# Performance work log

Measured on AMD Instinct MI355X. Metric: run time of the kernel, lower is better.

The kernel has to match this reference:

```python
import jax, jax.numpy as jnp
import numpy as np

B, N, DIM, VDIM, H, HD = 4, 1369, 1024, 1536, 16, 64
ROPE_HW, ROPE_DIM, THETA = 37, 32, 10000.0
LN_EPS = 1e-5


def _rope_tables():
    # VisionRotaryEmbeddingFast: freqs_for='lang', dim=32, pt_seq_len=ft_seq_len=37
    inv = 1.0 / THETA ** (jnp.arange(0, ROPE_DIM, 2, dtype=jnp.float32) / ROPE_DIM)  # [16]
    t = jnp.arange(ROPE_HW, dtype=jnp.float32) / ROPE_HW * ROPE_HW                    # [37]
    f = t[:, None] * inv[None, :]                                                     # [37,16]
    f = jnp.repeat(f, 2, axis=-1)                                                     # [37,32]
    # broadcat along last dim over the 2D grid -> [37,37,64]
    f2 = jnp.concatenate([jnp.broadcast_to(f[:, None, :], (ROPE_HW, ROPE_HW, ROPE_DIM)),
                          jnp.broadcast_to(f[None, :, :], (ROPE_HW, ROPE_HW, ROPE_DIM))], axis=-1)
    f2 = f2.reshape(-1, 2 * ROPE_DIM)                                                 # [1369,64]
    return jnp.cos(f2), jnp.sin(f2)


def _rotate_half(x):
    # pairs (x0,x1) -> (-x1,x0), interleaved
    xr = x.reshape(*x.shape[:-1], x.shape[-1] // 2, 2)
    x1, x2 = xr[..., 0], xr[..., 1]
    return jnp.stack((-x2, x1), axis=-1).reshape(x.shape)


def setup_inputs() -> dict:
    key = jax.random.key(0)
    ks = jax.random.split(key, 8)
    return {
        "x": jax.random.normal(ks[0], (B, N, DIM), jnp.float32),
        "value": jax.random.normal(ks[1], (B, N, VDIM), jnp.float32),
        "attn_mask": jax.random.randint(ks[2], (B, N), 0, 2).astype(bool),
        "wq": jax.random.normal(ks[3], (DIM, DIM), jnp.float32) * 0.02,
        "wk": jax.random.normal(ks[4], (DIM, VDIM), jnp.float32) * 0.02,
        "wv": jax.random.normal(ks[5], (DIM, VDIM), jnp.float32) * 0.02,
        "ln_g": jnp.ones((DIM,), jnp.float32),
        "ln_b": jnp.zeros((DIM,), jnp.float32),
        "wp": jax.random.normal(ks[6], (DIM, DIM), jnp.float32) * 0.02,
        "bp": jnp.zeros((DIM,), jnp.float32),
    }


def reference(x, value, attn_mask, wq, wk, wv, ln_g, ln_b, wp, bp):
    cos, sin = _rope_tables()  # [N, 64] each
    # projections (torch F.linear: y = x @ W.T)
    q = jnp.einsum('bni,oi->bno', x, wq).reshape(B, N, H, HD).transpose(0, 2, 1, 3)
    k = jnp.einsum('bni,oi->bno', value, wk).reshape(B, N, H, HD).transpose(0, 2, 1, 3)
    v = jnp.einsum('bni,oi->bno', value, wv).reshape(B, N, H, HD).transpose(0, 2, 1, 3)
    # inline RoPE on q and k
    q = q * cos + _rotate_half(q) * sin
    k = k * cos + _rotate_half(k) * sin
    q = q * (HD ** -0.5)
    attn = jnp.einsum('bhnd,bhmd->bhnm', q, k)
    neg_inf = jnp.finfo(attn.dtype).min
    attn = jnp.where(attn_mask[:, None, None, :], attn, neg_inf)
    attn = jax.nn.softmax(attn, axis=-1)
    out = jnp.einsum('bhnm,bhmd->bhnd', attn, v)
    out = out.transpose(0, 2, 1, 3).reshape(B, N, H * HD)
    # inner_attn_ln (LayerNorm, eps=1e-5)
    mu = jnp.mean(out, axis=-1, keepdims=True)
    var = jnp.var(out, axis=-1, keepdims=True)
    out = (out - mu) * jax.lax.rsqrt(var + LN_EPS) * ln_g + ln_b
    # output projection
    return jnp.einsum('bni,oi->bno', out, wp) + bp
```

## Files before the change

kernel.cpp:

```cpp
#include <hip/hip_runtime.h>
#include <hip/hip_bf16.h>

#define BB 4
#define NN 1369
#define DIMM 1024
#define VDIMM 1536
#define HH 16
#define MM (BB*NN)
#define MPAD 5504
#define NPAD 1408
#define KVB 64
#define NT (NPAD/KVB)
#define QSCALE 0.18028334f

typedef __attribute__((ext_vector_type(4))) float f32x4;
typedef __attribute__((ext_vector_type(8))) __bf16 bf16x8;
typedef __attribute__((ext_vector_type(4))) __bf16 bf16x4;

#define GLOAD_LDS(gsrc, ldst) \
  __builtin_amdgcn_global_load_lds((const __attribute__((address_space(1))) unsigned int*)(gsrc), \
                                   (__attribute__((address_space(3))) unsigned int*)(ldst), 16, 0, 0)

__global__ __launch_bounds__(256) void cvt_inputs(const float* __restrict__ x,
                                                  const float* __restrict__ val,
                                                  __bf16* __restrict__ xb,
                                                  __bf16* __restrict__ vb) {
  const int NX = MM * 1024 / 4;
  const int NV = MM * 1536 / 4;
  int i = blockIdx.x * blockDim.x + threadIdx.x;
  int st = gridDim.x * blockDim.x;
  for (; i < NX + NV; i += st) {
    const float* s; __bf16* d; int j;
    if (i < NX) { s = x; d = xb; j = i; }
    else        { s = val; d = vb; j = i - NX; }
    f32x4 v = ((const f32x4*)s)[j];
    bf16x4 o;
    o[0] = (__bf16)v[0]; o[1] = (__bf16)v[1];
    o[2] = (__bf16)v[2]; o[3] = (__bf16)v[3];
    ((bf16x4*)d)[j] = o;
  }
}

__global__ __launch_bounds__(256) void cvt_weights(
    const float* __restrict__ wq, const float* __restrict__ wk,
    const float* __restrict__ wv, const float* __restrict__ wp,
    const float* __restrict__ g,
    __bf16* __restrict__ wqb, __bf16* __restrict__ wkvb, __bf16* __restrict__ wgb) {
  const int NQ = 1024 * 1024 / 4;
  const int NK = 1024 * 1536 / 4;
  int i = blockIdx.x * blockDim.x + threadIdx.x;
  int st = gridDim.x * blockDim.x;
  for (; i < 2 * NQ + 2 * NK; i += st) {
    int j = i;
    if (j < NQ) {
      f32x4 v = ((const f32x4*)wq)[j];
      bf16x4 o;
      o[0] = (__bf16)v[0]; o[1] = (__bf16)v[1]; o[2] = (__bf16)v[2]; o[3] = (__bf16)v[3];
      ((bf16x4*)wqb)[j] = o;
    } else if (j < NQ + NK) {
      j -= NQ;
      f32x4 v = ((const f32x4*)wk)[j];
      bf16x4 o;
      o[0] = (__bf16)v[0]; o[1] = (__bf16)v[1]; o[2] = (__bf16)v[2]; o[3] = (__bf16)v[3];
      ((bf16x4*)wkvb)[j] = o;
    } else if (j < NQ + 2 * NK) {
      j -= NQ + NK;
      f32x4 v = ((const f32x4*)wv)[j];
      bf16x4 o;
      o[0] = (__bf16)v[0]; o[1] = (__bf16)v[1]; o[2] = (__bf16)v[2]; o[3] = (__bf16)v[3];
      ((bf16x4*)(wkvb + (size_t)1024 * 1536))[j] = o;
    } else {
      j -= NQ + 2 * NK;
      f32x4 v = ((const f32x4*)wp)[j];
      f32x4 gv = ((const f32x4*)g)[j & 255];
      bf16x4 o;
      o[0] = (__bf16)(v[0] * gv[0]); o[1] = (__bf16)(v[1] * gv[1]);
      o[2] = (__bf16)(v[2] * gv[2]); o[3] = (__bf16)(v[3] * gv[3]);
      ((bf16x4*)wgb)[j] = o;
    }
  }
}

__global__ __launch_bounds__(256) void c12_kernel(
    const float* __restrict__ wp, const float* __restrict__ g,
    const float* __restrict__ lnb, const float* __restrict__ bpv,
    float* __restrict__ c1, float* __restrict__ c2) {
  const int w = threadIdx.x >> 6, l = threadIdx.x & 63;
  const int o = blockIdx.x * 4 + w;
  const float* row = wp + (size_t)o * 1024;
  float s1 = 0.f, s2 = 0.f;
#pragma unroll
  for (int j = 0; j < 4; ++j) {
    const int idx = l * 4 + j * 256;
    f32x4 wv = *(const f32x4*)&row[idx];
    f32x4 gv = *(const f32x4*)&g[idx];
    f32x4 bv = *(const f32x4*)&lnb[idx];
#pragma unroll
    for (int e = 0; e < 4; ++e) { s1 += wv[e] * gv[e]; s2 += wv[e] * bv[e]; }
  }
#pragma unroll
  for (int m = 1; m < 64; m <<= 1) { s1 += __shfl_xor(s1, m); s2 += __shfl_xor(s2, m); }
  if (l == 0) { c1[o] = s1; c2[o] = s2 + bpv[o]; }
}

__global__ __launch_bounds__(256) void stats_kernel(
    const __bf16* __restrict__ AO, float* __restrict__ mu, float* __restrict__ rstd) {
  const int w = threadIdx.x >> 6, l = threadIdx.x & 63;
  const int row = blockIdx.x * 4 + w;
  const __bf16* x = AO + (size_t)row * DIMM + l * 16;
  float s = 0.f, sq = 0.f;
#pragma unroll
  for (int j = 0; j < 2; ++j) {
    bf16x8 v = *(const bf16x8*)&x[j * 8];
#pragma unroll
    for (int e = 0; e < 8; ++e) { float f = (float)v[e]; s += f; sq += f * f; }
  }
#pragma unroll
  for (int m = 1; m < 64; m <<= 1) { s += __shfl_xor(s, m); sq += __shfl_xor(sq, m); }
  if (l == 0) {
    float mean = s * (1.f / 1024.f);
    mu[row] = mean;
    rstd[row] = rsqrtf(sq * (1.f / 1024.f) - mean * mean + 1e-5f);
  }
}

__global__ __launch_bounds__(256) void prep_aux(float* __restrict__ cosT,
                                                float* __restrict__ sinT,
                                                const void* __restrict__ mask,
                                                float* __restrict__ maskA) {
  const int blk = blockIdx.x;
  if (blk < 343) {
    int idx = blk * 256 + threadIdx.x;
    if (idx >= NN * 64) return;
    int n = idx >> 6, d = idx & 63;
    int r = n / 37, c = n % 37;
    int m = (d < 32) ? (d >> 1) : ((d - 32) >> 1);
    float p = (d < 32) ? (float)r : (float)c;
    float inv = powf(10000.f, -(float)m * (1.f / 16.f));
    float a = p * inv;
    cosT[idx] = cosf(a);
    sinT[idx] = sinf(a);
  } else {
    __shared__ int flags[2];
    int t = threadIdx.x;
    if (t < 2) flags[t] = 0;
    __syncthreads();
    const unsigned int* mw = (const unsigned int*)mask;
    for (int i = t; i < NN; i += blockDim.x) {
      unsigned int w = mw[i];
      if (w == 0x3F800000u) atomicOr(&flags[1], 1);
      else if (w > 1u) atomicOr(&flags[0], 1);
    }
    __syncthreads();
    int md = flags[1] ? 2 : (flags[0] ? 1 : 0);
    const unsigned char* mb = (const unsigned char*)mask;
    const float* mf = (const float*)mask;
    for (int i = t; i < BB * NPAD; i += blockDim.x) {
      int b = i / NPAD, key = i % NPAD;
      float v = -1e30f;
      if (key < NN) {
        int idx = b * NN + key;
        bool on = (md == 0) ? (mw[idx] != 0u) : (md == 1) ? (mb[idx] != 0) : (mf[idx] != 0.f);
        if (on) v = 0.f;
      }
      maskA[i] = v;
    }
  }
}

template <int TN, int EPI, int GRID2D>
__global__ __launch_bounds__(256) void gemm_bt(
    const __bf16* __restrict__ A, const __bf16* __restrict__ W, int K,
    __bf16* __restrict__ obf, __bf16* __restrict__ obf2, float* __restrict__ of32,
    const float* __restrict__ cosT, const float* __restrict__ sinT,
    const float* __restrict__ mu, const float* __restrict__ rstd,
    const float* __restrict__ c1, const float* __restrict__ c2) {
  constexpr int MI = (TN == 128) ? 4 : 2;
  __shared__ __bf16 As[2][128 * 32];
  __shared__ __bf16 Bs[2][TN * 32];
  const int tid = threadIdx.x;
  const int w = tid >> 6, l = tid & 63;
  int tN, tM;
  if (GRID2D) {
    tN = blockIdx.x; tM = blockIdx.y;
  } else {
    const int i0 = blockIdx.x;
    const int orig = (i0 & 7) * 86 + (i0 >> 3);
    tN = orig & 15; tM = orig >> 4;
  }
  const int wm = (TN == 128) ? (w >> 1) : w;
  const int wn = (TN == 128) ? (w & 1) : 0;
  const int wmo = wm * ((TN == 128) ? 64 : 32);
  const int lo = l & 15, hi = l >> 4;

  const __bf16* Asrc = A + (size_t)(tM * 128 + lo) * K + hi * 8;
  const __bf16* Wsrc = W + (size_t)(tN * TN + lo) * K + hi * 8;

  f32x4 zero = {0.f, 0.f, 0.f, 0.f};
  f32x4 acc[MI][4];
#pragma unroll
  for (int i = 0; i < MI; ++i)
#pragma unroll
    for (int j = 0; j < 4; ++j) acc[i][j] = zero;

  auto GSTAGE = [&](int buf, int k0) {
#pragma unroll
    for (int j = 0; j < 2; ++j) {
      const int c = j * 4 + w;
      GLOAD_LDS(Asrc + (size_t)c * 16 * K + k0, (char*)&As[buf][c * 512]);
    }
    if constexpr (TN == 128) {
#pragma unroll
      for (int j = 0; j < 2; ++j) {
        const int c = j * 4 + w;
        GLOAD_LDS(Wsrc + (size_t)c * 16 * K + k0, (char*)&Bs[buf][c * 512]);
      }
    } else {
      GLOAD_LDS(Wsrc + (size_t)w * 16 * K + k0, (char*)&Bs[buf][w * 512]);
    }
  };

  const int nk = K >> 5;
  GSTAGE(0, 0);
  int cur = 0;
  const int ga = wmo >> 4;
  const int gb = (TN == 128) ? (wn * 4) : 0;
  for (int t = 0; t < nk; ++t) {
    __syncthreads();
    if (t + 1 < nk) GSTAGE(cur ^ 1, (t + 1) * 32);
    bf16x8 af[MI], bfr[4];
#pragma unroll
    for (int mi = 0; mi < MI; ++mi)
      af[mi] = *(const bf16x8*)&As[cur][(ga + mi) * 512 + hi * 128 + lo * 8];
#pragma unroll
    for (int ni = 0; ni < 4; ++ni)
      bfr[ni] = *(const bf16x8*)&Bs[cur][(gb + ni) * 512 + hi * 128 + lo * 8];
    __builtin_amdgcn_s_setprio(1);
#pragma unroll
    for (int mi = 0; mi < MI; ++mi)
#pragma unroll
      for (int ni = 0; ni < 4; ++ni)
        acc[mi][ni] = __builtin_amdgcn_mfma_f32_16x16x32_bf16(af[mi], bfr[ni], acc[mi][ni], 0, 0, 0);
    __builtin_amdgcn_s_setprio(0);
    cur ^= 1;
  }

  const int m_base = tM * 128 + wmo;
  const int o_base = tN * TN + wn * 64;
  const bool isK = (EPI == 1) && (tN < 8);
  float c1v[4], c2v[4];
  if (EPI == 3) {
#pragma unroll
    for (int ni = 0; ni < 4; ++ni) {
      c1v[ni] = c1[o_base + ni * 16 + lo];
      c2v[ni] = c2[o_base + ni * 16 + lo];
    }
  }
#pragma unroll
  for (int mi = 0; mi < MI; ++mi) {
    const int m4 = m_base + mi * 16 + hi * 4;
    if (EPI == 1 && !isK) {
      if (m4 < MM) {
        const int b0 = m4 / NN, n0 = m4 % NN;
#pragma unroll
        for (int ni = 0; ni < 4; ++ni) {
          const int o2 = o_base + ni * 16 + lo - 1024;
          const int h = o2 >> 6, d = o2 & 63;
          if (n0 <= NN - 4) {
            bf16x4 pv;
#pragma unroll
            for (int r = 0; r < 4; ++r) pv[r] = (__bf16)acc[mi][ni][r];
            *(bf16x4*)&obf2[((size_t)(b0 * HH + h) * 64 + d) * NPAD + n0] = pv;
          } else {
#pragma unroll
            for (int r = 0; r < 4; ++r) {
              const int mr = m4 + r;
              const int br = mr / NN, nr = mr % NN;
              obf2[((size_t)(br * HH + h) * 64 + d) * NPAD + nr] = (__bf16)acc[mi][ni][r];
            }
          }
        }
      }
    } else {
#pragma unroll
      for (int r = 0; r < 4; ++r) {
        const int mrow = m4 + r;
#pragma unroll
        for (int ni = 0; ni < 4; ++ni) {
          const int col = o_base + ni * 16 + lo;
          float v = acc[mi][ni][r];
          if (EPI == 0 || EPI == 1) {
            float pprt = __shfl_xor(v, 1);
            if (mrow < MM) {
              int b = mrow / NN, n = mrow % NN;
              int h = col >> 6, d = col & 63;
              float cs = cosT[n * 64 + d], sn = sinT[n * 64 + d];
              float out = v * cs + (((d & 1) == 0) ? -pprt : pprt) * sn;
              if (EPI == 0) out *= QSCALE;
              obf[((size_t)(b * HH + h) * NPAD + n) * 64 + d] = (__bf16)out;
            }
          } else {
            if (mrow < MM)
              of32[(size_t)mrow * DIMM + col] =
                  rstd[mrow] * (v - mu[mrow] * c1v[ni]) + c2v[ni];
          }
        }
      }
    }
  }
}

__device__ inline unsigned int pk2(float a, float b) {
  unsigned int ua = (unsigned int)__builtin_bit_cast(unsigned short, (__bf16)a);
  unsigned int ub = (unsigned int)__builtin_bit_cast(unsigned short, (__bf16)b);
  return ua | (ub << 16);
}

__global__ __launch_bounds__(256) void attn_kernel(
    const __bf16* __restrict__ Qb, const __bf16* __restrict__ Kb,
    const __bf16* __restrict__ Vtb, const float* __restrict__ maskA,
    __bf16* __restrict__ AO) {
  __shared__ __bf16 Ks[2][64 * 64];
  __shared__ __bf16 Vs[2][64 * 64];
  __shared__ unsigned int Plds[4][16 * 32];
  const int tid = threadIdx.x;
  const int w = tid >> 6, l = tid & 63;
  const int lo = l & 15, hi = l >> 4;

  const int i = blockIdx.x;
  const int orig = (i & 7) * 176 + (i >> 3);
  const int bh = orig / NT;
  const int qt = orig % NT;
  const int b = bh >> 4;
  const int q0 = qt * 64 + w * 16;

  const __bf16* Qp = Qb + ((size_t)bh * NPAD + q0) * 64;
  bf16x8 qf0 = *(const bf16x8*)&Qp[lo * 64 + hi * 8];
  bf16x8 qf1 = *(const bf16x8*)&Qp[lo * 64 + 32 + hi * 8];

  const int row8 = l >> 3;
  const int swz16 = ((l & 7) ^ row8) << 4;
  const int lo7 = lo & 7;
  const int swzW = (lo & 7) << 2;

  f32x4 zero = {0.f, 0.f, 0.f, 0.f};
  f32x4 O[4];
#pragma unroll
  for (int n = 0; n < 4; ++n) O[n] = zero;
  float lr = 0.f;
  const float* mk = maskA + b * NPAD;

#define STAGE(buf, k0)                                                                   \
  {                                                                                      \
    _Pragma("unroll") for (int j = 0; j < 2; ++j) {                                      \
      const int rbase = (j * 4 + w) * 8;                                                 \
      const char* ksrc = (const char*)Kb +                                               \
          ((size_t)bh * NPAD + (k0) + rbase + row8) * 128 + swz16;                       \
      GLOAD_LDS(ksrc, (char*)&Ks[buf][0] + rbase * 128);                                 \
      const char* vsrc = (const char*)Vtb +                                              \
          ((size_t)(bh * 64 + rbase + row8) * NPAD + (k0)) * 2 + swz16;                  \
      GLOAD_LDS(vsrc, (char*)&Vs[buf][0] + rbase * 128);                                 \
    }                                                                                    \
  }

  STAGE(0, 0);
  __syncthreads();
  int cur = 0;

  for (int t = 0; t < NT; ++t) {
    if (t + 1 < NT) STAGE(cur ^ 1, (t + 1) * KVB);

    const __bf16* KB = &Ks[cur][0];
    const __bf16* VB = &Vs[cur][0];

    f32x4 mv[4];
#pragma unroll
    for (int c = 0; c < 4; ++c) mv[c] = *(const f32x4*)&mk[t * KVB + c * 16 + hi * 4];

    f32x4 S[4];
    __builtin_amdgcn_s_setprio(1);
#pragma unroll
    for (int c = 0; c < 4; ++c) {
      const int kr = c * 16 + lo;
      bf16x8 kfa = *(const bf16x8*)&KB[kr * 64 + ((hi ^ lo7) * 8)];
      bf16x8 kfb = *(const bf16x8*)&KB[kr * 64 + (((hi + 4) ^ lo7) * 8)];
      f32x4 s = __builtin_amdgcn_mfma_f32_16x16x32_bf16(kfa, qf0, zero, 0, 0, 0);
      S[c]     = __builtin_amdgcn_mfma_f32_16x16x32_bf16(kfb, qf1, s, 0, 0, 0);
    }
    __builtin_amdgcn_s_setprio(0);

    float rs = 0.f;
#pragma unroll
    for (int c = 0; c < 4; ++c) {
      float p0 = exp2f(S[c][0] + mv[c][0]);
      float p1 = exp2f(S[c][1] + mv[c][1]);
      float p2 = exp2f(S[c][2] + mv[c][2]);
      float p3 = exp2f(S[c][3] + mv[c][3]);
      rs += (p0 + p1) + (p2 + p3);
      uint2 pw = {pk2(p0, p1), pk2(p2, p3)};
      *(uint2*)&Plds[w][lo * 32 + ((8 * c + 2 * hi) ^ swzW)] = pw;
    }
    lr += rs;

    bf16x8 pf0 = *(const bf16x8*)&Plds[w][lo * 32 + ((4 * hi) ^ swzW)];
    bf16x8 pf1 = *(const bf16x8*)&Plds[w][lo * 32 + ((16 + 4 * hi) ^ swzW)];

    __builtin_amdgcn_s_setprio(1);
#pragma unroll
    for (int n = 0; n < 4; ++n) {
      const int vr = n * 16 + lo;
      bf16x8 vfa = *(const bf16x8*)&VB[vr * 64 + ((hi ^ lo7) * 8)];
      bf16x8 vfb = *(const bf16x8*)&VB[vr * 64 + (((hi + 4) ^ lo7) * 8)];
      O[n] = __builtin_amdgcn_mfma_f32_16x16x32_bf16(vfa, pf0, O[n], 0, 0, 0);
      O[n] = __builtin_amdgcn_mfma_f32_16x16x32_bf16(vfb, pf1, O[n], 0, 0, 0);
    }
    __builtin_amdgcn_s_setprio(0);

    __syncthreads();
    cur ^= 1;
  }
#undef STAGE

  lr += __shfl_xor(lr, 16);
  lr += __shfl_xor(lr, 32);
  const float inv = 1.f / lr;

  const int h = bh & 15;
  const int token = q0 + lo;
  if (token < NN) {
    __bf16* dst = AO + (size_t)(b * NN + token) * DIMM + h * 64 + hi * 4;
#pragma unroll
    for (int n = 0; n < 4; ++n) {
      bf16x4 o;
#pragma unroll
      for (int e = 0; e < 4; ++e) o[e] = (__bf16)(O[n][e] * inv);
      *(bf16x4*)(dst + n * 16) = o;
    }
  }
}

extern "C" void kernel_launch(void* const* d_in, const int* in_sizes, int n_in,
                              void* d_out, int out_size, void* d_ws, size_t ws_size,
                              hipStream_t stream) {
  const float* x   = (const float*)d_in[0];
  const float* val = (const float*)d_in[1];
  const void*  msk = d_in[2];
  const float* wq  = (const float*)d_in[3];
  const float* wk  = (const float*)d_in[4];
  const float* wv  = (const float*)d_in[5];
  const float* lng = (const float*)d_in[6];
  const float* lnb = (const float*)d_in[7];
  const float* wp  = (const float*)d_in[8];
  const float* bpv = (const float*)d_in[9];
  float* out = (float*)d_out;

  char* ws = (char*)d_ws;
  size_t off = 0;
  auto alloc = [&](size_t bytes) -> char* {
    char* p = ws + off;
    off += (bytes + 255) & ~(size_t)255;
    return p;
  };
  __bf16* xb   = (__bf16*)alloc((size_t)MPAD * 1024 * 2);
  __bf16* vb   = (__bf16*)alloc((size_t)MPAD * 1536 * 2);
  __bf16* wqb  = (__bf16*)alloc((size_t)1024 * 1024 * 2);
  __bf16* wkvb = (__bf16*)alloc((size_t)2048 * 1536 * 2);
  __bf16* wgb  = (__bf16*)alloc((size_t)1024 * 1024 * 2);
  __bf16* Qb   = (__bf16*)alloc((size_t)64 * NPAD * 64 * 2);
  __bf16* Kb   = (__bf16*)alloc((size_t)64 * NPAD * 64 * 2);
  __bf16* Vtb  = (__bf16*)alloc((size_t)64 * 64 * NPAD * 2);
  __bf16* AO   = (__bf16*)alloc((size_t)MPAD * 1024 * 2);
  float* cosT  = (float*)alloc((size_t)NN * 64 * 4);
  float* sinT  = (float*)alloc((size_t)NN * 64 * 4);
  float* maskA = (float*)alloc((size_t)BB * NPAD * 4);
  float* muv   = (float*)alloc((size_t)MM * 4);
  float* rstdv = (float*)alloc((size_t)MM * 4);
  float* c1v   = (float*)alloc((size_t)1024 * 4);
  float* c2v   = (float*)alloc((size_t)1024 * 4);


  cvt_inputs<<<2048, 256, 0, stream>>>(x, val, xb, vb);
  cvt_weights<<<1024, 256, 0, stream>>>(wq, wk, wv, wp, lng, wqb, wkvb, wgb);
  prep_aux<<<344, 256, 0, stream>>>(cosT, sinT, msk, maskA);
  c12_kernel<<<256, 256, 0, stream>>>(wp, lng, lnb, bpv, c1v, c2v);

  gemm_bt<64, 0, 1><<<dim3(16, 43), 256, 0, stream>>>(xb, wqb, 1024, Qb, nullptr, nullptr,
                                                      cosT, sinT, nullptr, nullptr, nullptr, nullptr);
  gemm_bt<128, 1, 0><<<dim3(688), 256, 0, stream>>>(vb, wkvb, 1536, Kb, Vtb, nullptr,
                                                    cosT, sinT, nullptr, nullptr, nullptr, nullptr);

  attn_kernel<<<dim3(64 * NT), 256, 0, stream>>>(Qb, Kb, Vtb, maskA, AO);

  stats_kernel<<<MM / 4, 256, 0, stream>>>(AO, muv, rstdv);

  gemm_bt<64, 3, 1><<<dim3(16, 43), 256, 0, stream>>>(AO, wgb, 1024, nullptr, nullptr, out,
                                                      nullptr, nullptr, muv, rstdv, c1v, c2v);
}
```

Measured before the change: 277.1 us.

## Use dedicated 256x256-tile, 4-stage pipelined GEMM for fused K/V projection

Replaces the 128x128-tile K/V projection GEMM with a dedicated kernel using 256x256 tiles, 512 threads and a 4-buffer LDS ring. Loads are issued two stages ahead, and explicit vmcnt waits are paired with a raw barrier. The larger tile increases reuse of each loaded A/W fragment, and the deeper prefetch hides global latency. In exchange it uses 128KB of LDS and more accumulator registers, and produces only 176 blocks, which may underfill 256 CUs. The padded value buffer grows to 5632 rows so the 256-row tiles stay in bounds.

Measured after the change: 263.1 us. -5.0%, faster.

```diff
diff --git a/kernel.cpp b/kernel.cpp
--- a/kernel.cpp
+++ b/kernel.cpp
@@ -8,6 +8,7 @@
 #define HH 16
 #define MM (BB*NN)
 #define MPAD 5504
+#define MPAD2 5632
 #define NPAD 1408
 #define KVB 64
 #define NT (NPAD/KVB)
@@ -168,98 +169,70 @@
   }
 }
 
-template <int TN, int EPI, int GRID2D>
-__global__ __launch_bounds__(256) void gemm_bt(
-    const __bf16* __restrict__ A, const __bf16* __restrict__ W, int K,
-    __bf16* __restrict__ obf, __bf16* __restrict__ obf2, float* __restrict__ of32,
-    const float* __restrict__ cosT, const float* __restrict__ sinT,
-    const float* __restrict__ mu, const float* __restrict__ rstd,
-    const float* __restrict__ c1, const float* __restrict__ c2) {
-  constexpr int MI = (TN == 128) ? 4 : 2;
-  __shared__ __bf16 As[2][128 * 32];
-  __shared__ __bf16 Bs[2][TN * 32];
+__global__ __launch_bounds__(512, 2) void gemm_kv256(
+    const __bf16* __restrict__ A, const __bf16* __restrict__ W,
+    __bf16* __restrict__ Kb, __bf16* __restrict__ Vtb,
+    const float* __restrict__ cosT, const float* __restrict__ sinT) {
+  __shared__ __bf16 Ar[4][256 * 32];
+  __shared__ __bf16 Br[4][256 * 32];
   const int tid = threadIdx.x;
-  const int w = tid >> 6, l = tid & 63;
-  int tN, tM;
-  if (GRID2D) {
-    tN = blockIdx.x; tM = blockIdx.y;
-  } else {
-    const int i0 = blockIdx.x;
-    const int orig = (i0 & 7) * 86 + (i0 >> 3);
-    tN = orig & 15; tM = orig >> 4;
-  }
-  const int wm = (TN == 128) ? (w >> 1) : w;
-  const int wn = (TN == 128) ? (w & 1) : 0;
-  const int wmo = wm * ((TN == 128) ? 64 : 32);
+  const int wid = tid >> 6, l = tid & 63;
+  const int wr = wid >> 2, wc = wid & 3;
   const int lo = l & 15, hi = l >> 4;
-
-  const __bf16* Asrc = A + (size_t)(tM * 128 + lo) * K + hi * 8;
-  const __bf16* Wsrc = W + (size_t)(tN * TN + lo) * K + hi * 8;
+  const int tN = blockIdx.x & 7, tM = blockIdx.x >> 3;
+  const int K = VDIMM;
+  const int nk = K / 32;
+
+  const int srow = (tid >> 6) * 16 + (tid & 15);
+  const int schunk = ((tid >> 4) & 3) * 8;
+  const __bf16* Asrc = A + (size_t)(tM * 256 + srow) * K + schunk;
+  const __bf16* Wsrc = W + (size_t)(tN * 256 + srow) * K + schunk;
 
   f32x4 zero = {0.f, 0.f, 0.f, 0.f};
-  f32x4 acc[MI][4];
-#pragma unroll
-  for (int i = 0; i < MI; ++i)
+  f32x4 acc[8][4];
+#pragma unroll
+  for (int i = 0; i < 8; ++i)
 #pragma unroll
     for (int j = 0; j < 4; ++j) acc[i][j] = zero;
 
-  auto GSTAGE = [&](int buf, int k0) {
-#pragma unroll
-    for (int j = 0; j < 2; ++j) {
-      const int c = j * 4 + w;
-      GLOAD_LDS(Asrc + (size_t)c * 16 * K + k0, (char*)&As[buf][c * 512]);
-    }
-    if constexpr (TN == 128) {
-#pragma unroll
-      for (int j = 0; j < 2; ++j) {
-        const int c = j * 4 + w;
-        GLOAD_LDS(Wsrc + (size_t)c * 16 * K + k0, (char*)&Bs[buf][c * 512]);
-      }
-    } else {
-      GLOAD_LDS(Wsrc + (size_t)w * 16 * K + k0, (char*)&Bs[buf][w * 512]);
-    }
+  auto GSTAGE = [&](int s, int k0) {
+    GLOAD_LDS(Asrc + k0,                (char*)&Ar[s][0] + tid * 16);
+    GLOAD_LDS(Asrc + (size_t)128 * K + k0, (char*)&Ar[s][0] + tid * 16 + 8192);
+    GLOAD_LDS(Wsrc + k0,                (char*)&Br[s][0] + tid * 16);
+    GLOAD_LDS(Wsrc + (size_t)128 * K + k0, (char*)&Br[s][0] + tid * 16 + 8192);
   };
 
-  const int nk = K >> 5;
   GSTAGE(0, 0);
-  int cur = 0;
-  const int ga = wmo >> 4;
-  const int gb = (TN == 128) ? (wn * 4) : 0;
+  GSTAGE(1, 32);
   for (int t = 0; t < nk; ++t) {
-    __syncthreads();
-    if (t + 1 < nk) GSTAGE(cur ^ 1, (t + 1) * 32);
-    bf16x8 af[MI], bfr[4];
-#pragma unroll
-    for (int mi = 0; mi < MI; ++mi)
-      af[mi] = *(const bf16x8*)&As[cur][(ga + mi) * 512 + hi * 128 + lo * 8];
+    if (t < nk - 1) asm volatile("s_waitcnt vmcnt(4)" ::: "memory");
+    else            asm volatile("s_waitcnt vmcnt(0)" ::: "memory");
+    __builtin_amdgcn_s_barrier();
+    const int s = t & 3;
+    bf16x8 af[8], bf[4];
+#pragma unroll
+    for (int mi = 0; mi < 8; ++mi)
+      af[mi] = *(const bf16x8*)&Ar[s][(wr * 8 + mi) * 512 + hi * 128 + lo * 8];
 #pragma unroll
     for (int ni = 0; ni < 4; ++ni)
-      bfr[ni] = *(const bf16x8*)&Bs[cur][(gb + ni) * 512 + hi * 128 + lo * 8];
+      bf[ni] = *(const bf16x8*)&Br[s][(wc * 4 + ni) * 512 + hi * 128 + lo * 8];
+    if (t + 2 < nk) GSTAGE((t + 2) & 3, (t + 2) * 32);
     __builtin_amdgcn_s_setprio(1);
 #pragma unroll
-    for (int mi = 0; mi < MI; ++mi)
+    for (int mi = 0; mi < 8; ++mi)
 #pragma unroll
       for (int ni = 0; ni < 4; ++ni)
-        acc[mi][ni] = __builtin_amdgcn_mfma_f32_16x16x32_bf16(af[mi], bfr[ni], acc[mi][ni], 0, 0, 0);
+        acc[mi][ni] = __builtin_amdgcn_mfma_f32_16x16x32_bf16(af[mi], bf[ni], acc[mi][ni], 0, 0, 0);
     __builtin_amdgcn_s_setprio(0);
-    cur ^= 1;
-  }
-
-  const int m_base = tM * 128 + wmo;
-  const int o_base = tN * TN + wn * 64;
-  const bool isK = (EPI == 1) && (tN < 8);
-  float c1v[4], c2v[4];
-  if (EPI == 3) {
-#pragma unroll
-    for (int ni = 0; ni < 4; ++ni) {
-      c1v[ni] = c1[o_base + ni * 16 + lo];
-      c2v[ni] = c2[o_base + ni * 16 + lo];
-    }
-  }
-#pragma unroll
-  for (int mi = 0; mi < MI; ++mi) {
+  }
+
+  const int m_base = tM * 256 + wr * 128;
+  const int o_base = tN * 256 + wc * 64;
+  const bool isK = (tN < 4);
+#pragma unroll
+  for (int mi = 0; mi < 8; ++mi) {
     const int m4 = m_base + mi * 16 + hi * 4;
-    if (EPI == 1 && !isK) {
+    if (!isK) {
       if (m4 < MM) {
         const int b0 = m4 / NN, n0 = m4 % NN;
 #pragma unroll
@@ -270,13 +243,13 @@
             bf16x4 pv;
 #pragma unroll
             for (int r = 0; r < 4; ++r) pv[r] = (__bf16)acc[mi][ni][r];
-            *(bf16x4*)&obf2[((size_t)(b0 * HH + h) * 64 + d) * NPAD + n0] = pv;
+            *(bf16x4*)&Vtb[((size_t)(b0 * HH + h) * 64 + d) * NPAD + n0] = pv;
           } else {
 #pragma unroll
             for (int r = 0; r < 4; ++r) {
               const int mr = m4 + r;
               const int br = mr / NN, nr = mr % NN;
-              obf2[((size_t)(br * HH + h) * 64 + d) * NPAD + nr] = (__bf16)acc[mi][ni][r];
+              Vtb[((size_t)(br * HH + h) * 64 + d) * NPAD + nr] = (__bf16)acc[mi][ni][r];
             }
           }
         }
@@ -289,21 +262,110 @@
         for (int ni = 0; ni < 4; ++ni) {
           const int col = o_base + ni * 16 + lo;
           float v = acc[mi][ni][r];
-          if (EPI == 0 || EPI == 1) {
-            float pprt = __shfl_xor(v, 1);
-            if (mrow < MM) {
-              int b = mrow / NN, n = mrow % NN;
-              int h = col >> 6, d = col & 63;
-              float cs = cosT[n * 64 + d], sn = sinT[n * 64 + d];
-              float out = v * cs + (((d & 1) == 0) ? -pprt : pprt) * sn;
-              if (EPI == 0) out *= QSCALE;
-              obf[((size_t)(b * HH + h) * NPAD + n) * 64 + d] = (__bf16)out;
-            }
-          } else {
-            if (mrow < MM)
-              of32[(size_t)mrow * DIMM + col] =
-                  rstd[mrow] * (v - mu[mrow] * c1v[ni]) + c2v[ni];
+          float pprt = __shfl_xor(v, 1);
+          if (mrow < MM) {
+            int b = mrow / NN, n = mrow % NN;
+            int h = col >> 6, d = col & 63;
+            float cs = cosT[n * 64 + d], sn = sinT[n * 64 + d];
+            float out = v * cs + (((d & 1) == 0) ? -pprt : pprt) * sn;
+            Kb[((size_t)(b * HH + h) * NPAD + n) * 64 + d] = (__bf16)out;
           }
+        }
+      }
+    }
+  }
+}
+
+template <int EPI>
+__global__ __launch_bounds__(256) void gemm_bt(
+    const __bf16* __restrict__ A, const __bf16* __restrict__ W, int K,
+    __bf16* __restrict__ obf, float* __restrict__ of32,
+    const float* __restrict__ cosT, const float* __restrict__ sinT,
+    const float* __restrict__ mu, const float* __restrict__ rstd,
+    const float* __restrict__ c1, const float* __restrict__ c2) {
+  __shared__ __bf16 As[2][128 * 32];
+  __shared__ __bf16 Bs[2][64 * 32];
+  const int tid = threadIdx.x;
+  const int w = tid >> 6, l = tid & 63;
+  const int tN = blockIdx.x, tM = blockIdx.y;
+  const int wmo = w * 32;
+  const int lo = l & 15, hi = l >> 4;
+
+  const __bf16* Asrc = A + (size_t)(tM * 128 + lo) * K + hi * 8;
+  const __bf16* Wsrc = W + (size_t)(tN * 64 + lo) * K + hi * 8;
+
+  f32x4 zero = {0.f, 0.f, 0.f, 0.f};
+  f32x4 acc[2][4];
+#pragma unroll
+  for (int i = 0; i < 2; ++i)
+#pragma unroll
+    for (int j = 0; j < 4; ++j) acc[i][j] = zero;
+
+  auto GSTAGE = [&](int buf, int k0) {
+#pragma unroll
+    for (int j = 0; j < 2; ++j) {
+      const int c = j * 4 + w;
+      GLOAD_LDS(Asrc + (size_t)c * 16 * K + k0, (char*)&As[buf][c * 512]);
+    }
+    GLOAD_LDS(Wsrc + (size_t)w * 16 * K + k0, (char*)&Bs[buf][w * 512]);
+  };
+
+  const int nk = K >> 5;
+  GSTAGE(0, 0);
+  int cur = 0;
+  const int ga = wmo >> 4;
+  for (int t = 0; t < nk; ++t) {
+    __syncthreads();
+    if (t + 1 < nk) GSTAGE(cur ^ 1, (t + 1) * 32);
+    bf16x8 af[2], bfr[4];
+#pragma unroll
+    for (int mi = 0; mi < 2; ++mi)
+      af[mi] = *(const bf16x8*)&As[cur][(ga + mi) * 512 + hi * 128 + lo * 8];
+#pragma unroll
+    for (int ni = 0; ni < 4; ++ni)
+      bfr[ni] = *(const bf16x8*)&Bs[cur][ni * 512 + hi * 128 + lo * 8];
+    __builtin_amdgcn_s_setprio(1);
+#pragma unroll
+    for (int mi = 0; mi < 2; ++mi)
+#pragma unroll
+      for (int ni = 0; ni < 4; ++ni)
+        acc[mi][ni] = __builtin_amdgcn_mfma_f32_16x16x32_bf16(af[mi], bfr[ni], acc[mi][ni], 0, 0, 0);
+    __builtin_amdgcn_s_setprio(0);
+    cur ^= 1;
+  }
+
+  const int m_base = tM * 128 + wmo;
+  const int o_base = tN * 64;
+  float c1v[4], c2v[4];
+  if (EPI == 3) {
+#pragma unroll
+    for (int ni = 0; ni < 4; ++ni) {
+      c1v[ni] = c1[o_base + ni * 16 + lo];
+      c2v[ni] = c2[o_base + ni * 16 + lo];
+    }
+  }
+#pragma unroll
+  for (int mi = 0; mi < 2; ++mi) {
+#pragma unroll
+    for (int r = 0; r < 4; ++r) {
+      const int mrow = m_base + mi * 16 + hi * 4 + r;
+#pragma unroll
+      for (int ni = 0; ni < 4; ++ni) {
+        const int col = o_base + ni * 16 + lo;
+        float v = acc[mi][ni][r];
+        if (EPI == 0) {
+          float pprt = __shfl_xor(v, 1);
+          if (mrow < MM) {
+            int b = mrow / NN, n = mrow % NN;
+            int h = col >> 6, d = col & 63;
+            float cs = cosT[n * 64 + d], sn = sinT[n * 64 + d];
+            float out = (v * cs + (((d & 1) == 0) ? -pprt : pprt) * sn) * QSCALE;
+            obf[((size_t)(b * HH + h) * NPAD + n) * 64 + d] = (__bf16)out;
+          }
+        } else {
+          if (mrow < MM)
+            of32[(size_t)mrow * DIMM + col] =
+                rstd[mrow] * (v - mu[mrow] * c1v[ni]) + c2v[ni];
         }
       }
     }
@@ -462,7 +524,7 @@
     return p;
   };
   __bf16* xb   = (__bf16*)alloc((size_t)MPAD * 1024 * 2);
-  __bf16* vb   = (__bf16*)alloc((size_t)MPAD * 1536 * 2);
+  __bf16* vb   = (__bf16*)alloc((size_t)MPAD2 * 1536 * 2);
   __bf16* wqb  = (__bf16*)alloc((size_t)1024 * 1024 * 2);
   __bf16* wkvb = (__bf16*)alloc((size_t)2048 * 1536 * 2);
   __bf16* wgb  = (__bf16*)alloc((size_t)1024 * 1024 * 2);
@@ -484,15 +546,14 @@
   prep_aux<<<344, 256, 0, stream>>>(cosT, sinT, msk, maskA);
   c12_kernel<<<256, 256, 0, stream>>>(wp, lng, lnb, bpv, c1v, c2v);
 
-  gemm_bt<64, 0, 1><<<dim3(16, 43), 256, 0, stream>>>(xb, wqb, 1024, Qb, nullptr, nullptr,
-                                                      cosT, sinT, nullptr, nullptr, nullptr, nullptr);
-  gemm_bt<128, 1, 0><<<dim3(688), 256, 0, stream>>>(vb, wkvb, 1536, Kb, Vtb, nullptr,
-                                                    cosT, sinT, nullptr, nullptr, nullptr, nullptr);
+  gemm_bt<0><<<dim3(16, 43), 256, 0, stream>>>(xb, wqb, 1024, Qb, nullptr,
+                                               cosT, sinT, nullptr, nullptr, nullptr, nullptr);
+  gemm_kv256<<<dim3(176), 512, 0, stream>>>(vb, wkvb, Kb, Vtb, cosT, sinT);
 
   attn_kernel<<<dim3(64 * NT), 256, 0, stream>>>(Qb, Kb, Vtb, maskA, AO);
 
   stats_kernel<<<MM / 4, 256, 0, stream>>>(AO, muv, rstdv);
 
-  gemm_bt<64, 3, 1><<<dim3(16, 43), 256, 0, stream>>>(AO, wgb, 1024, nullptr, nullptr, out,
-                                                      nullptr, nullptr, muv, rstdv, c1v, c2v);
-}
+  gemm_bt<3><<<dim3(16, 43), 256, 0, stream>>>(AO, wgb, 1024, nullptr, out,
+                                               nullptr, nullptr, muv, rstdv, c1v, c2v);
+}
```
